# Performance work log

Hardware: AMD Instinct MI355X
Metric: run time of the kernel (lower is better)

The kernel has to match this reference:

```python
import jax, jax.numpy as jnp
import numpy as np

N = 50000      # nodes
E = 800000     # edges
F = 256        # input features (glove identity)
H = 64         # hidden dim of GCN stack
C = 16         # num classes
PE = 200000    # pos/neg edges each

@jax.custom_vjp
def grad_reverse(x):
    return x

def _gr_fwd(x):
    return x, None

def _gr_bwd(_, g):
    return (-g,)

grad_reverse.defvjp(_gr_fwd, _gr_bwd)

def _gcn_norm(edge_index, n):
    # add self loops + symmetric normalization (PyG GCNConv default)
    loops = jnp.arange(n, dtype=edge_index.dtype)
    src = jnp.concatenate([edge_index[0], loops])
    dst = jnp.concatenate([edge_index[1], loops])
    deg = jax.ops.segment_sum(jnp.ones(src.shape, jnp.float32), dst, num_segments=n)
    dinv = jnp.where(deg > 0, jax.lax.rsqrt(jnp.maximum(deg, 1.0)), 0.0)
    return src, dst, dinv[src] * dinv[dst]

def _gcn(x, W, b, src, dst, norm, n):
    h = x @ W                                   # [n, out]
    msg = h[src] * norm[:, None]                # gather + edge scale
    return jax.ops.segment_sum(msg, dst, num_segments=n) + b

def setup_inputs():
    key = jax.random.key(0)
    ks = jax.random.split(key, 14)
    s = 0.05
    return {
        "input": jax.random.normal(ks[0], (N, F), jnp.float32),
        "glove": jnp.eye(F, dtype=jnp.float32),
        "W1": jax.random.normal(ks[1], (F, H), jnp.float32) * s,
        "b1": jnp.zeros((H,), jnp.float32),
        "W2": jax.random.normal(ks[2], (H, H), jnp.float32) * s,
        "b2": jnp.zeros((H,), jnp.float32),
        "W3": jax.random.normal(ks[3], (H, H), jnp.float32) * s,
        "b3": jnp.zeros((H,), jnp.float32),
        "Wa": jax.random.normal(ks[4], (H, C), jnp.float32) * s,
        "ba": jnp.zeros((C,), jnp.float32),
        "Wk": jax.random.normal(ks[5], (H, C), jnp.float32) * s,
        "bk": jnp.zeros((C,), jnp.float32),
        "edge_index": jax.random.randint(ks[6], (2, E), 0, N, dtype=jnp.int32),
        "pos_edge_index": jax.random.randint(ks[7], (2, PE), 0, N, dtype=jnp.int32),
        "neg_edge_index": jax.random.randint(ks[8], (2, PE), 0, N, dtype=jnp.int32),
    }

def reference(input, glove, W1, b1, W2, b2, W3, b3, Wa, ba, Wk, bk,
              edge_index, pos_edge_index, neg_edge_index):
    src, dst, norm = _gcn_norm(edge_index, N)
    x = input @ glove
    x = jax.nn.relu(_gcn(x, W1, b1, src, dst, norm, N))
    x = _gcn(x, W2, b2, src, dst, norm, N)
    x = _gcn(x, W3, b3, src, dst, norm, N)
    feat = x
    attr = _gcn(x, Wa, ba, src, dst, norm, N)
    att = _gcn(grad_reverse(x), Wk, bk, src, dst, norm, N)
    tei = jnp.concatenate([pos_edge_index, neg_edge_index], axis=-1)  # [2, 2*PE]
    x_j = x[tei[0]]
    x_i = x[tei[1]]
    res = jnp.einsum('ef,ef->e', x_i, x_j)
    return res, jax.nn.log_softmax(attr, axis=1), att, feat
```

## Files before the change

kernel.cpp:

```cpp
#include <hip/hip_runtime.h>
#include <hip/hip_bf16.h>

#define N_NODES 50000
#define N_EDGES 800000
#define F_IN    256
#define H_DIM   64
#define C_DIM   16
#define PE_CNT  200000

typedef __hip_bfloat16 bf16;

__device__ __forceinline__ float b2f(bf16 v) { return __bfloat162float(v); }
__device__ __forceinline__ bf16  f2b(float v) { return __float2bfloat16(v); }


__global__ void hist_build_kernel(const int* __restrict__ dst, int* __restrict__ hist,
                                  const float* __restrict__ Wa, const float* __restrict__ Wk,
                                  float* __restrict__ Wh) {
    int e = blockIdx.x * blockDim.x + threadIdx.x;
    if (e < N_EDGES) atomicAdd(&hist[dst[e]], 1);
    if (blockIdx.x == 0) {
        for (int idx = threadIdx.x; idx < H_DIM * 32; idx += 256) {
            int f = idx >> 5, c = idx & 31;
            Wh[idx] = (c < C_DIM) ? Wa[f * C_DIM + c] : Wk[f * C_DIM + (c - C_DIM)];
        }
    }
}

__global__ __launch_bounds__(1024) void scan_block_kernel(const int* __restrict__ hist,
                                                          int* __restrict__ excl,
                                                          int* __restrict__ partials) {
    __shared__ int buf[1024];
    int i = blockIdx.x * 1024 + threadIdx.x;
    int v = (i < N_NODES) ? hist[i] : 0;
    buf[threadIdx.x] = v;
    __syncthreads();
    for (int off = 1; off < 1024; off <<= 1) {
        int t = (threadIdx.x >= off) ? buf[threadIdx.x - off] : 0;
        __syncthreads();
        buf[threadIdx.x] += t;
        __syncthreads();
    }
    int incl = buf[threadIdx.x];
    if (i < N_NODES) excl[i] = incl - v;
    if (threadIdx.x == 1023) partials[blockIdx.x] = incl;
}

__global__ void scan_partials_kernel(int* __restrict__ partials) {
    int t = threadIdx.x;
    int orig = (t < 49) ? partials[t] : 0;
    int v = orig;
    for (int off = 1; off < 64; off <<= 1) {
        int u = __shfl_up(v, off, 64);
        if (t >= off) v += u;
    }
    if (t < 49) partials[t] = v - orig;
}

__global__ void scan_add_kernel(int* __restrict__ rowstart, const int* __restrict__ partials,
                                int* __restrict__ cursor, const int* __restrict__ hist,
                                float* __restrict__ dinv) {
    int i = blockIdx.x * blockDim.x + threadIdx.x;
    if (i < N_NODES) {
        int v = rowstart[i] + partials[i >> 10];
        rowstart[i] = v;
        cursor[i]   = v;
        dinv[i]     = rsqrtf((float)(hist[i] + 1));
    } else if (i == N_NODES) {
        rowstart[i] = N_EDGES;
    }
}

__global__ void scatter_kernel(const int* __restrict__ ei, int* __restrict__ cursor,
                               const float* __restrict__ dinv, int2* __restrict__ csr2) {
    int e = blockIdx.x * blockDim.x + threadIdx.x;
    if (e < N_EDGES) {
        int s = ei[e];
        int d = ei[N_EDGES + e];
        int p = atomicAdd(&cursor[d], 1);
        csr2[p] = make_int2(s, __float_as_int(dinv[s]));
    }
}

__global__ __launch_bounds__(256) void gemm_k256_kernel(const float* __restrict__ x,
                                                        const float* __restrict__ W,
                                                        bf16* __restrict__ h1) {
    int col = threadIdx.x & 63;
    int wid = __builtin_amdgcn_readfirstlane(threadIdx.x >> 6);
    int row0 = blockIdx.x * 64 + wid * 16;
    if (row0 >= N_NODES) return;
    const float* xp = x + (size_t)row0 * F_IN;
    float acc[16];
#pragma unroll
    for (int i = 0; i < 16; i++) acc[i] = 0.f;
    for (int k = 0; k < F_IN; k += 4) {
        float w0 = W[(k + 0) * H_DIM + col];
        float w1 = W[(k + 1) * H_DIM + col];
        float w2 = W[(k + 2) * H_DIM + col];
        float w3 = W[(k + 3) * H_DIM + col];
#pragma unroll
        for (int i = 0; i < 16; i++) {
            acc[i] += xp[i * F_IN + k + 0] * w0;
            acc[i] += xp[i * F_IN + k + 1] * w1;
            acc[i] += xp[i * F_IN + k + 2] * w2;
            acc[i] += xp[i * F_IN + k + 3] * w3;
        }
    }
#pragma unroll
    for (int i = 0; i < 16; i++)
        h1[(size_t)(row0 + i) * H_DIM + col] = f2b(acc[i]);
}

template <int RELU>
__global__ __launch_bounds__(256) void agg_gemm_kernel(const bf16* __restrict__ h,
                                                       const int* __restrict__ rowstart,
                                                       const int2* __restrict__ csr2,
                                                       const float* __restrict__ dinv,
                                                       const float* __restrict__ bagg,
                                                       const float* __restrict__ W,
                                                       bf16* __restrict__ hnext) {
    int lane = threadIdx.x & 63;
    int node = blockIdx.x * 4 + __builtin_amdgcn_readfirstlane(threadIdx.x >> 6);
    float dn = dinv[node];
    int s0 = rowstart[node], s1 = rowstart[node + 1];
    float acc0 = dn * b2f(h[(size_t)node * H_DIM + lane]);
    float acc1 = 0.f;
    int j = s0;
    for (; j + 1 < s1; j += 2) {
        int2 e0 = csr2[j], e1 = csr2[j + 1];
        acc0 += __int_as_float(e0.y) * b2f(h[(size_t)e0.x * H_DIM + lane]);
        acc1 += __int_as_float(e1.y) * b2f(h[(size_t)e1.x * H_DIM + lane]);
    }
    if (j < s1) {
        int2 e0 = csr2[j];
        acc0 += __int_as_float(e0.y) * b2f(h[(size_t)e0.x * H_DIM + lane]);
    }
    float v = dn * (acc0 + acc1) + bagg[lane];
    if (RELU) v = fmaxf(v, 0.f);
    float o = 0.f;
#pragma unroll
    for (int f = 0; f < H_DIM; f++) {
        float vf = __shfl(v, f, 64);
        o += vf * W[f * H_DIM + lane];
    }
    hnext[(size_t)node * H_DIM + lane] = f2b(o);
}

__global__ __launch_bounds__(256) void agg_out_kernel(const bf16* __restrict__ h,
                                                      const int* __restrict__ rowstart,
                                                      const int2* __restrict__ csr2,
                                                      const float* __restrict__ dinv,
                                                      const float* __restrict__ b3,
                                                      float* __restrict__ feat,
                                                      bf16* __restrict__ featb) {
    int lane = threadIdx.x & 63;
    int node = blockIdx.x * 4 + __builtin_amdgcn_readfirstlane(threadIdx.x >> 6);
    float dn = dinv[node];
    int s0 = rowstart[node], s1 = rowstart[node + 1];
    float acc0 = dn * b2f(h[(size_t)node * H_DIM + lane]);
    float acc1 = 0.f;
    int j = s0;
    for (; j + 1 < s1; j += 2) {
        int2 e0 = csr2[j], e1 = csr2[j + 1];
        acc0 += __int_as_float(e0.y) * b2f(h[(size_t)e0.x * H_DIM + lane]);
        acc1 += __int_as_float(e1.y) * b2f(h[(size_t)e1.x * H_DIM + lane]);
    }
    if (j < s1) {
        int2 e0 = csr2[j];
        acc0 += __int_as_float(e0.y) * b2f(h[(size_t)e0.x * H_DIM + lane]);
    }
    float v = dn * (acc0 + acc1) + b3[lane];
    feat[(size_t)node * H_DIM + lane]  = v;
    featb[(size_t)node * H_DIM + lane] = f2b(v);
}

__global__ __launch_bounds__(256) void head_kernel(const bf16* __restrict__ featb,
                                                   const int* __restrict__ rowstart,
                                                   const int2* __restrict__ csr2,
                                                   const float* __restrict__ dinv,
                                                   const float* __restrict__ Wh,
                                                   const float* __restrict__ ba,
                                                   const float* __restrict__ bk,
                                                   float* __restrict__ lsm,
                                                   float* __restrict__ att) {
    int lane = threadIdx.x & 63;
    int node = blockIdx.x * 4 + __builtin_amdgcn_readfirstlane(threadIdx.x >> 6);
    float dn = dinv[node];
    int s0 = rowstart[node], s1 = rowstart[node + 1];
    float acc0 = dn * b2f(featb[(size_t)node * H_DIM + lane]);
    float acc1 = 0.f;
    int j = s0;
    for (; j + 1 < s1; j += 2) {
        int2 e0 = csr2[j], e1 = csr2[j + 1];
        acc0 += __int_as_float(e0.y) * b2f(featb[(size_t)e0.x * H_DIM + lane]);
        acc1 += __int_as_float(e1.y) * b2f(featb[(size_t)e1.x * H_DIM + lane]);
    }
    if (j < s1) {
        int2 e0 = csr2[j];
        acc0 += __int_as_float(e0.y) * b2f(featb[(size_t)e0.x * H_DIM + lane]);
    }
    float y = dn * (acc0 + acc1);

    int c32 = lane & 31;
    int fbase = lane & 32;
    float part = 0.f;
#pragma unroll
    for (int i = 0; i < 32; i++) {
        float yf = __shfl(y, fbase + i, 64);
        part += yf * Wh[(fbase + i) * 32 + c32];
    }
    float full = part + __shfl(part, lane ^ 32, 64);
    if (lane < 32) {
        float bias = (lane < C_DIM) ? ba[lane] : bk[lane - C_DIM];
        float hv = full + bias;
        if (lane < C_DIM) {
            float m = hv;
#pragma unroll
            for (int off = 1; off < 16; off <<= 1) m = fmaxf(m, __shfl_xor(m, off, 64));
            float e = __expf(hv - m);
            float sum = e;
#pragma unroll
            for (int off = 1; off < 16; off <<= 1) sum += __shfl_xor(sum, off, 64);
            lsm[(size_t)node * C_DIM + lane] = (hv - m) - __logf(sum);
        } else {
            att[(size_t)node * C_DIM + (lane - C_DIM)] = hv;
        }
    }
}

__global__ __launch_bounds__(256) void edge_dot_kernel(const int* __restrict__ pos,
                                                       const int* __restrict__ neg,
                                                       const bf16* __restrict__ xb,
                                                       float* __restrict__ res) {
    int e = blockIdx.x * 16 + (threadIdx.x >> 4);
    int lane = threadIdx.x & 15;
    int a, b;
    if (e < PE_CNT) {
        a = pos[e];
        b = pos[PE_CNT + e];
    } else {
        int e2 = e - PE_CNT;
        a = neg[e2];
        b = neg[PE_CNT + e2];
    }
    uint2 ua = ((const uint2*)(xb + (size_t)a * H_DIM))[lane];
    uint2 ub = ((const uint2*)(xb + (size_t)b * H_DIM))[lane];
    float a0 = __uint_as_float(ua.x << 16), a1 = __uint_as_float(ua.x & 0xffff0000u);
    float a2 = __uint_as_float(ua.y << 16), a3 = __uint_as_float(ua.y & 0xffff0000u);
    float b0 = __uint_as_float(ub.x << 16), b1 = __uint_as_float(ub.x & 0xffff0000u);
    float b2 = __uint_as_float(ub.y << 16), b3 = __uint_as_float(ub.y & 0xffff0000u);
    float acc = a0 * b0 + a1 * b1 + a2 * b2 + a3 * b3;
#pragma unroll
    for (int off = 1; off < 16; off <<= 1) acc += __shfl_xor(acc, off, 64);
    if (lane == 0) res[e] = acc;
}


extern "C" void kernel_launch(void* const* d_in, const int* in_sizes, int n_in,
                              void* d_out, int out_size, void* d_ws, size_t ws_size,
                              hipStream_t stream) {
    const float* input = (const float*)d_in[0];
    const float* W1 = (const float*)d_in[2];
    const float* b1 = (const float*)d_in[3];
    const float* W2 = (const float*)d_in[4];
    const float* b2 = (const float*)d_in[5];
    const float* W3 = (const float*)d_in[6];
    const float* b3 = (const float*)d_in[7];
    const float* Wa = (const float*)d_in[8];
    const float* ba = (const float*)d_in[9];
    const float* Wk = (const float*)d_in[10];
    const float* bk = (const float*)d_in[11];
    const int* ei  = (const int*)d_in[12];
    const int* pos = (const int*)d_in[13];
    const int* neg = (const int*)d_in[14];

    char* ws = (char*)d_ws;
    int*   hist     = (int*)(ws + 0);
    int*   rowstart = (int*)(ws + 200704);
    int*   cursor   = (int*)(ws + 401408);
    float* dinv     = (float*)(ws + 602112);
    int*   partials = (int*)(ws + 802816);
    float* Wh       = (float*)(ws + 803072);
    int2*  csr2     = (int2*)(ws + 811264);
    bf16*  bufA     = (bf16*)(ws + 7211264ULL);
    bf16*  bufB     = (bf16*)(ws + 13611264ULL);

    float* out  = (float*)d_out;
    float* res  = out;
    float* lsm  = out + 400000;
    float* att  = out + 1200000;
    float* feat = out + 2000000;

    hipMemsetAsync(hist, 0, N_NODES * sizeof(int), stream);
    hist_build_kernel<<<(N_EDGES + 255) / 256, 256, 0, stream>>>(ei + N_EDGES, hist, Wa, Wk, Wh);
    scan_block_kernel<<<49, 1024, 0, stream>>>(hist, rowstart, partials);
    scan_partials_kernel<<<1, 64, 0, stream>>>(partials);
    scan_add_kernel<<<196, 256, 0, stream>>>(rowstart, partials, cursor, hist, dinv);
    scatter_kernel<<<(N_EDGES + 255) / 256, 256, 0, stream>>>(ei, cursor, dinv, csr2);

    gemm_k256_kernel<<<782, 256, 0, stream>>>(input, W1, bufA);
    agg_gemm_kernel<1><<<12500, 256, 0, stream>>>(bufA, rowstart, csr2, dinv, b1, W2, bufB);
    agg_gemm_kernel<0><<<12500, 256, 0, stream>>>(bufB, rowstart, csr2, dinv, b2, W3, bufA);
    agg_out_kernel<<<12500, 256, 0, stream>>>(bufA, rowstart, csr2, dinv, b3, feat, bufB);
    head_kernel<<<12500, 256, 0, stream>>>(bufB, rowstart, csr2, dinv, Wh, ba, bk, lsm, att);
    edge_dot_kernel<<<25000, 256, 0, stream>>>(pos, neg, bufB, res);
}
```

Before: 542.9 us.

## Tile first-layer GEMM through shared memory with coalesced float4 loads

Rewrites the 50000x256 by 256x64 input GEMM so each block stages a 32-row slab of x and a 64-row chunk of W1 in LDS using coalesced float4 global loads. Rows are then read from LDS as float4, with padding to limit bank conflicts. The old version had each wave read x rows with per-lane broadcast scalar loads straight from global memory. The change also makes blocks smaller and more numerous (1563 instead of 782), adds bounds checks for the tail rows, and adds two barriers per K chunk.

```diff
diff --git a/kernel.cpp b/kernel.cpp
--- a/kernel.cpp
+++ b/kernel.cpp
@@ -82,33 +82,66 @@
     }
 }
 
+#define G_ROWS 32
+#define G_KCH  64
+#define XS_LD  68
+
 __global__ __launch_bounds__(256) void gemm_k256_kernel(const float* __restrict__ x,
                                                         const float* __restrict__ W,
                                                         bf16* __restrict__ h1) {
-    int col = threadIdx.x & 63;
-    int wid = __builtin_amdgcn_readfirstlane(threadIdx.x >> 6);
-    int row0 = blockIdx.x * 64 + wid * 16;
-    if (row0 >= N_NODES) return;
-    const float* xp = x + (size_t)row0 * F_IN;
-    float acc[16];
-#pragma unroll
-    for (int i = 0; i < 16; i++) acc[i] = 0.f;
-    for (int k = 0; k < F_IN; k += 4) {
-        float w0 = W[(k + 0) * H_DIM + col];
-        float w1 = W[(k + 1) * H_DIM + col];
-        float w2 = W[(k + 2) * H_DIM + col];
-        float w3 = W[(k + 3) * H_DIM + col];
-#pragma unroll
-        for (int i = 0; i < 16; i++) {
-            acc[i] += xp[i * F_IN + k + 0] * w0;
-            acc[i] += xp[i * F_IN + k + 1] * w1;
-            acc[i] += xp[i * F_IN + k + 2] * w2;
-            acc[i] += xp[i * F_IN + k + 3] * w3;
-        }
-    }
-#pragma unroll
-    for (int i = 0; i < 16; i++)
-        h1[(size_t)(row0 + i) * H_DIM + col] = f2b(acc[i]);
+    __shared__ float xs[G_ROWS * XS_LD];
+    __shared__ float ws[G_KCH * H_DIM];
+    int t = threadIdx.x;
+    int row0 = blockIdx.x * G_ROWS;
+    int col = t & 63;
+    int wv  = t >> 6;
+
+    float acc[8];
+#pragma unroll
+    for (int i = 0; i < 8; i++) acc[i] = 0.f;
+
+    for (int c = 0; c < F_IN / G_KCH; c++) {
+        int k0 = c * G_KCH;
+        {
+            const float4* Wg = (const float4*)(W + k0 * H_DIM);
+            float4* wl = (float4*)ws;
+#pragma unroll
+            for (int i = 0; i < 4; i++) wl[t + 256 * i] = Wg[t + 256 * i];
+        }
+        {
+            int r = t >> 3;
+            int jj = (t & 7) * 8;
+            int row = row0 + r;
+            float4 v0 = make_float4(0.f, 0.f, 0.f, 0.f), v1 = v0;
+            if (row < N_NODES) {
+                const float4* xg = (const float4*)(x + (size_t)row * F_IN + k0 + jj);
+                v0 = xg[0];
+                v1 = xg[1];
+            }
+            float4* xl = (float4*)&xs[r * XS_LD + jj];
+            xl[0] = v0;
+            xl[1] = v1;
+        }
+        __syncthreads();
+#pragma unroll 4
+        for (int kk = 0; kk < G_KCH; kk += 4) {
+            float w0 = ws[(kk + 0) * H_DIM + col];
+            float w1 = ws[(kk + 1) * H_DIM + col];
+            float w2 = ws[(kk + 2) * H_DIM + col];
+            float w3 = ws[(kk + 3) * H_DIM + col];
+#pragma unroll
+            for (int i = 0; i < 8; i++) {
+                float4 xv = *(const float4*)&xs[(wv * 8 + i) * XS_LD + kk];
+                acc[i] += xv.x * w0 + xv.y * w1 + xv.z * w2 + xv.w * w3;
+            }
+        }
+        __syncthreads();
+    }
+#pragma unroll
+    for (int i = 0; i < 8; i++) {
+        int row = row0 + wv * 8 + i;
+        if (row < N_NODES) h1[(size_t)row * H_DIM + col] = f2b(acc[i]);
+    }
 }
 
 template <int RELU>
@@ -298,7 +331,7 @@
     scan_add_kernel<<<196, 256, 0, stream>>>(rowstart, partials, cursor, hist, dinv);
     scatter_kernel<<<(N_EDGES + 255) / 256, 256, 0, stream>>>(ei, cursor, dinv, csr2);
 
-    gemm_k256_kernel<<<782, 256, 0, stream>>>(input, W1, bufA);
+    gemm_k256_kernel<<<(N_NODES + G_ROWS - 1) / G_ROWS, 256, 0, stream>>>(input, W1, bufA);
     agg_gemm_kernel<1><<<12500, 256, 0, stream>>>(bufA, rowstart, csr2, dinv, b1, W2, bufB);
     agg_gemm_kernel<0><<<12500, 256, 0, stream>>>(bufB, rowstart, csr2, dinv, b2, W3, bufA);
     agg_out_kernel<<<12500, 256, 0, stream>>>(bufA, rowstart, csr2, dinv, b3, feat, bufB);
```

After: 437.0 us. -19.5%, faster.
